# Performance work log

Hardware: AMD Instinct MI355X
Metric: run time of the kernel (lower is better)

Reference implementation:

```python
import jax, jax.numpy as jnp
import numpy as np

EPS = 1e-8  # torch CosineSimilarity default eps


def setup_inputs() -> dict:
    key = jax.random.key(0)
    ks = jax.random.split(key, 9)
    B, C, H, W = 8, 256, 96, 96
    co = C // 2
    s = 0.05
    return {
        "x": jax.random.normal(ks[0], (B, C, H, W), dtype=jnp.float32),
        "w_theta": jax.random.normal(ks[1], (co, C), dtype=jnp.float32) * s,
        "b_theta": jax.random.normal(ks[2], (co,), dtype=jnp.float32) * s,
        "w_phi": jax.random.normal(ks[3], (co, C), dtype=jnp.float32) * s,
        "b_phi": jax.random.normal(ks[4], (co,), dtype=jnp.float32) * s,
        "w_g": jax.random.normal(ks[5], (co, C), dtype=jnp.float32) * s,
        "b_g": jax.random.normal(ks[6], (co,), dtype=jnp.float32) * s,
        "w_back": jax.random.normal(ks[7], (C, co), dtype=jnp.float32) * s,
        "b_back": jax.random.normal(ks[8], (C,), dtype=jnp.float32) * s,
    }


def reference(x, w_theta, b_theta, w_phi, b_phi, w_g, b_g, w_back, b_back):
    B, C, H, W = x.shape
    # replicate pad, then gather the 9 (3x3) shifted views: [B, C, 9, H, W]
    xp = jnp.pad(x, ((0, 0), (0, 0), (1, 1), (1, 1)), mode="edge")
    neigh = jnp.stack(
        [xp[:, :, i:i + H, j:j + W] for i in range(3) for j in range(3)], axis=2
    )
    # 1x1 convs are per-pixel linear maps
    theta = jnp.einsum("bchw,oc->bohw", x, w_theta) + b_theta[None, :, None, None]
    phi = jnp.einsum("bcnhw,oc->bonhw", neigh, w_phi) + b_phi[None, :, None, None, None]
    g = jnp.einsum("bcnhw,oc->bonhw", neigh, w_g) + b_g[None, :, None, None, None]
    # cosine similarity over channel dim o: [B, 9, H, W]
    dot = jnp.sum(phi * theta[:, :, None], axis=1)
    denom = jnp.maximum(
        jnp.sqrt(jnp.sum(phi * phi, axis=1)) * jnp.sqrt(jnp.sum(theta * theta, axis=1))[:, None],
        EPS,
    )
    attn = jax.nn.softmax(dot / denom, axis=1)  # softmax over 9 neighbors
    # weighted average of g over neighbors: [B, co, H, W]
    wa = jnp.einsum("bonhw,bnhw->bohw", g, attn)
    x_res = jnp.einsum("bohw,co->bchw", wa, w_back) + b_back[None, :, None, None]
    return x + x_res
```

## Files before the change

### kernel.cpp

```cpp
#include <hip/hip_runtime.h>
#include <hip/hip_bf16.h>
#include <math.h>

#define HW   9216
#define WIMG 96
#define NPIX 73728
#define CIN  256
#define CO   128

typedef __attribute__((ext_vector_type(8))) short short8v;
typedef __attribute__((ext_vector_type(8))) unsigned short u16x8;
typedef __attribute__((ext_vector_type(4))) float f32x4;

__device__ __forceinline__ unsigned short f2bf(float f) {
    __hip_bfloat16 h = __float2bfloat16(f);
    return __builtin_bit_cast(unsigned short, h);
}
__device__ __forceinline__ float bf2f(unsigned short u) {
    unsigned v = ((unsigned)u) << 16;
    return __builtin_bit_cast(float, v);
}

__device__ __forceinline__ int swz(int row, int kb) {
    return (row * 128) + (kb ^ ((row & 7) << 4));
}
__device__ __forceinline__ int swzA(int row, int kb) {
    return (row * 512) + (kb ^ ((row & 7) << 4));
}

__global__ __launch_bounds__(256) void k1_mfma(
    const float* __restrict__ x,
    const float* __restrict__ wt, const float* __restrict__ bt,
    const float* __restrict__ wp, const float* __restrict__ bp,
    const float* __restrict__ wg, const float* __restrict__ bg,
    unsigned short* __restrict__ th, unsigned short* __restrict__ ph,
    unsigned short* __restrict__ gf)
{
    __shared__ char As[128 * 512];
    __shared__ char Bs[128 * 128];

    const int t   = threadIdx.x;
    const int bid = blockIdx.x;
    const int lb  = (bid & 7) * 72 + (bid >> 3);
    const int P0  = lb * 128;
    const int b   = P0 / HW;
    const int p0  = P0 - b * HW;
    const float* xb = x + (size_t)b * CIN * HW + p0;

    const int wid = t >> 6, lane = t & 63;
    const int wm = (wid & 1) * 64, wn = (wid >> 1) * 64;
    const int l15 = lane & 15, lg = lane >> 4;

    for (int kt = 0; kt < CIN; kt += 64) {
        #pragma unroll
        for (int it = 0; it < 8; ++it) {
            int kq = ((t >> 4) & 3) + (it & 3) * 4;
            int pp = (t & 15) + ((t >> 6) << 4) + ((it >> 2) << 6);
            ushort4 v;
            v.x = f2bf(xb[(size_t)(kt + kq * 4 + 0) * HW + pp]);
            v.y = f2bf(xb[(size_t)(kt + kq * 4 + 1) * HW + pp]);
            v.z = f2bf(xb[(size_t)(kt + kq * 4 + 2) * HW + pp]);
            v.w = f2bf(xb[(size_t)(kt + kq * 4 + 3) * HW + pp]);
            *(ushort4*)(As + swzA(pp, (kt + kq * 4) * 2)) = v;
        }
    }

    for (int nb = 0; nb < 3; ++nb) {
        const float* W  = (nb == 0) ? wt : (nb == 1) ? wp : wg;
        const float* Bv = (nb == 0) ? bt : (nb == 1) ? bp : bg;
        unsigned short* O = (nb == 0) ? th : (nb == 1) ? ph : gf;

        f32x4 acc[4][4] = {};

        for (int kt = 0; kt < CIN; kt += 64) {
            __syncthreads();
            #pragma unroll
            for (int it = 0; it < 8; ++it) {
                int kq = t & 15;
                int n  = (t >> 4) + it * 16;
                float4 w4 = *(const float4*)(W + (size_t)n * CIN + kt + kq * 4);
                ushort4 v;
                v.x = f2bf(w4.x); v.y = f2bf(w4.y); v.z = f2bf(w4.z); v.w = f2bf(w4.w);
                *(ushort4*)(Bs + swz(n, kq * 8)) = v;
            }
            __syncthreads();
            #pragma unroll
            for (int ks = 0; ks < 2; ++ks) {
                const int akb = kt * 2 + ks * 64 + lg * 16;
                const int bkb = ks * 64 + lg * 16;
                short8v a[4], bq[4];
                #pragma unroll
                for (int mt = 0; mt < 4; ++mt)
                    a[mt] = *(const short8v*)(As + swzA(wm + mt * 16 + l15, akb));
                #pragma unroll
                for (int nt = 0; nt < 4; ++nt)
                    bq[nt] = *(const short8v*)(Bs + swz(wn + nt * 16 + l15, bkb));
                #pragma unroll
                for (int mt = 0; mt < 4; ++mt)
                    #pragma unroll
                    for (int nt = 0; nt < 4; ++nt)
                        acc[mt][nt] = __builtin_amdgcn_mfma_f32_16x16x32_bf16(
                            a[mt], bq[nt], acc[mt][nt], 0, 0, 0);
            }
        }

        float bias[4];
        #pragma unroll
        for (int nt = 0; nt < 4; ++nt) bias[nt] = Bv[wn + nt * 16 + l15];
        #pragma unroll
        for (int mt = 0; mt < 4; ++mt)
            #pragma unroll
            for (int j = 0; j < 4; ++j) {
                size_t row = (size_t)(P0 + wm + mt * 16 + lg * 4 + j) * CO;
                #pragma unroll
                for (int nt = 0; nt < 4; ++nt)
                    O[row + wn + nt * 16 + l15] = f2bf(acc[mt][nt][j] + bias[nt]);
            }
    }
}

__global__ __launch_bounds__(256) void k_attn(
    const unsigned short* __restrict__ th, const unsigned short* __restrict__ ph,
    const unsigned short* __restrict__ gf, unsigned short* __restrict__ wa)
{
    const int t   = threadIdx.x;
    const int bid = blockIdx.x;
    const int lb  = (bid & 7) * 144 + (bid >> 3);
    const int s = t >> 2, q = t & 3;
    const int P = lb * 64 + s;
    const int b = P / HW;
    const int p = P - b * HW;
    const int h = p / WIMG;
    const int w = p - h * WIMG;
    const size_t ib = (size_t)b * HW;

    size_t nbase[9];
    #pragma unroll
    for (int n = 0; n < 9; ++n) {
        int hh = h + n / 3 - 1; hh = hh < 0 ? 0 : (hh > 95 ? 95 : hh);
        int w2 = w + n % 3 - 1; w2 = w2 < 0 ? 0 : (w2 > 95 ? 95 : w2);
        nbase[n] = (ib + (size_t)hh * WIMG + w2) * CO + q * 32;
    }

    const u16x8* tv = (const u16x8*)(th + (size_t)P * CO + q * 32);
    float T32[32];
    #pragma unroll
    for (int j = 0; j < 4; ++j) {
        u16x8 v = tv[j];
        #pragma unroll
        for (int e = 0; e < 8; ++e) T32[j * 8 + e] = bf2f(v[e]);
    }
    float t4[4] = {0.f, 0.f, 0.f, 0.f};
    #pragma unroll
    for (int j = 0; j < 4; ++j)
        #pragma unroll
        for (int e = 0; e < 8; ++e)
            t4[j] = fmaf(T32[j * 8 + e], T32[j * 8 + e], t4[j]);
    float tt = (t4[0] + t4[1]) + (t4[2] + t4[3]);
    tt += __shfl_xor(tt, 1);
    tt += __shfl_xor(tt, 2);
    const float st = sqrtf(tt);

    float score[9];
    #pragma unroll
    for (int n = 0; n < 9; ++n) {
        const u16x8* pv = (const u16x8*)(ph + nbase[n]);
        float d4[4] = {0.f, 0.f, 0.f, 0.f};
        float p4[4] = {0.f, 0.f, 0.f, 0.f};
        #pragma unroll
        for (int j = 0; j < 4; ++j) {
            u16x8 v = pv[j];
            #pragma unroll
            for (int e = 0; e < 8; ++e) {
                float f = bf2f(v[e]);
                d4[j] = fmaf(T32[j * 8 + e], f, d4[j]);
                p4[j] = fmaf(f, f, p4[j]);
            }
        }
        float d  = (d4[0] + d4[1]) + (d4[2] + d4[3]);
        float pp = (p4[0] + p4[1]) + (p4[2] + p4[3]);
        d  += __shfl_xor(d, 1);  d  += __shfl_xor(d, 2);
        pp += __shfl_xor(pp, 1); pp += __shfl_xor(pp, 2);
        float den = fmaxf(sqrtf(pp) * st, 1e-8f);
        score[n] = d / den;
    }

    float mx = score[0];
    #pragma unroll
    for (int n = 1; n < 9; ++n) mx = fmaxf(mx, score[n]);
    float sum = 0.f;
    #pragma unroll
    for (int n = 0; n < 9; ++n) { score[n] = __expf(score[n] - mx); sum += score[n]; }
    const float inv = 1.f / sum;

    float acc[32];
    #pragma unroll
    for (int k = 0; k < 32; ++k) acc[k] = 0.f;

    #pragma unroll
    for (int n = 0; n < 9; ++n) {
        const u16x8* gv = (const u16x8*)(gf + nbase[n]);
        float a = score[n] * inv;
        #pragma unroll
        for (int j = 0; j < 4; ++j) {
            u16x8 v = gv[j];
            #pragma unroll
            for (int e = 0; e < 8; ++e)
                acc[j * 8 + e] = fmaf(a, bf2f(v[e]), acc[j * 8 + e]);
        }
    }

    u16x8* ov = (u16x8*)(wa + (size_t)P * CO + q * 32);
    #pragma unroll
    for (int j = 0; j < 4; ++j) {
        u16x8 o;
        #pragma unroll
        for (int e = 0; e < 8; ++e) o[e] = f2bf(acc[j * 8 + e]);
        ov[j] = o;
    }
}

__global__ __launch_bounds__(256) void k3_mfma(
    const unsigned short* __restrict__ wa, const float* __restrict__ wb,
    const float* __restrict__ bb_, const float* __restrict__ x,
    float* __restrict__ out)
{
    __shared__ char As[128 * 128];
    __shared__ char Bs[128 * 128];

    const int t   = threadIdx.x;
    const int bid = blockIdx.x;
    const int lb  = (bid & 7) * 144 + (bid >> 3);
    const int cb  = (lb & 1) * 128;
    const int P0  = (lb >> 1) * 128;
    const int b   = P0 / HW;
    const int p0  = P0 - b * HW;

    const int wid = t >> 6, lane = t & 63;
    const int wm = (wid & 1) * 64, wn = (wid >> 1) * 64;
    const int l15 = lane & 15, lg = lane >> 4;

    f32x4 acc[4][4] = {};

    for (int kt = 0; kt < CO; kt += 64) {
        if (kt) __syncthreads();
        #pragma unroll
        for (int it = 0; it < 8; ++it) {
            int kq = t & 15;
            int n  = (t >> 4) + it * 16;
            float4 w4 = *(const float4*)(wb + (size_t)(cb + n) * CO + kt + kq * 4);
            ushort4 v;
            v.x = f2bf(w4.x); v.y = f2bf(w4.y); v.z = f2bf(w4.z); v.w = f2bf(w4.w);
            *(ushort4*)(As + swz(n, kq * 8)) = v;
        }
        #pragma unroll
        for (int it = 0; it < 4; ++it) {
            int kq = t & 7;
            int n  = (t >> 3) + it * 32;
            u16x8 u = *(const u16x8*)(wa + (size_t)(P0 + n) * CO + kt + kq * 8);
            *(u16x8*)(Bs + swz(n, kq * 16)) = u;
        }
        __syncthreads();
        #pragma unroll
        for (int ks = 0; ks < 2; ++ks) {
            const int kk2 = ks * 64 + lg * 16;
            short8v a[4], bq[4];
            #pragma unroll
            for (int mt = 0; mt < 4; ++mt)
                a[mt] = *(const short8v*)(As + swz(wm + mt * 16 + l15, kk2));
            #pragma unroll
            for (int nt = 0; nt < 4; ++nt)
                bq[nt] = *(const short8v*)(Bs + swz(wn + nt * 16 + l15, kk2));
            #pragma unroll
            for (int mt = 0; mt < 4; ++mt)
                #pragma unroll
                for (int nt = 0; nt < 4; ++nt)
                    acc[mt][nt] = __builtin_amdgcn_mfma_f32_16x16x32_bf16(
                        a[mt], bq[nt], acc[mt][nt], 0, 0, 0);
        }
    }

    #pragma unroll
    for (int mt = 0; mt < 4; ++mt)
        #pragma unroll
        for (int j = 0; j < 4; ++j) {
            int ch = cb + wm + mt * 16 + lg * 4 + j;
            size_t base = ((size_t)b * CIN + ch) * HW + p0;
            float bias = bb_[ch];
            #pragma unroll
            for (int nt = 0; nt < 4; ++nt) {
                int px = wn + nt * 16 + l15;
                out[base + px] = x[base + px] + acc[mt][nt][j] + bias;
            }
        }
}

extern "C" void kernel_launch(void* const* d_in, const int* in_sizes, int n_in,
                              void* d_out, int out_size, void* d_ws, size_t ws_size,
                              hipStream_t stream)
{
    const float* x  = (const float*)d_in[0];
    const float* wt = (const float*)d_in[1];
    const float* bt = (const float*)d_in[2];
    const float* wp = (const float*)d_in[3];
    const float* bp = (const float*)d_in[4];
    const float* wg = (const float*)d_in[5];
    const float* bg = (const float*)d_in[6];
    const float* wb = (const float*)d_in[7];
    const float* bb = (const float*)d_in[8];
    float* out = (float*)d_out;

    const size_t FEAT = (size_t)NPIX * CO;
    unsigned short* th = (unsigned short*)d_ws;
    unsigned short* ph = th + FEAT;
    unsigned short* gf = ph + FEAT;
    unsigned short* wa = gf + FEAT;

    hipLaunchKernelGGL(k1_mfma, dim3(576), dim3(256), 0, stream,
                       x, wt, bt, wp, bp, wg, bg, th, ph, gf);
    hipLaunchKernelGGL(k_attn, dim3(1152), dim3(256), 0, stream,
                       th, ph, gf, wa);
    hipLaunchKernelGGL(k3_mfma, dim3(1152), dim3(256), 0, stream,
                       wa, wb, bb, x, out);
}
```

Baseline: 256.3 us.

## Split projection kernel per weight matrix and use transposed LDS reads for x

The first kernel now launches one block per (pixel tile, projection) pair instead of one block computing all three projections, which cuts LDS use from 80 KB to 32 KB and triples the grid for better occupancy. x is loaded with vectorized float4 reads in pixel-major layout, and the MFMA A operands are fetched with ds_read_b64_tr_b16 transposed LDS reads. The cost is that each x tile is read and converted three times, once per projection, though the repeats should mostly be served from cache.

```diff
diff --git a/kernel.cpp b/kernel.cpp
--- a/kernel.cpp
+++ b/kernel.cpp
@@ -11,6 +11,7 @@
 typedef __attribute__((ext_vector_type(8))) short short8v;
 typedef __attribute__((ext_vector_type(8))) unsigned short u16x8;
 typedef __attribute__((ext_vector_type(4))) float f32x4;
+typedef __attribute__((ext_vector_type(4))) unsigned u32x4;
 
 __device__ __forceinline__ unsigned short f2bf(float f) {
     __hip_bfloat16 h = __float2bfloat16(f);
@@ -24,8 +25,12 @@
 __device__ __forceinline__ int swz(int row, int kb) {
     return (row * 128) + (kb ^ ((row & 7) << 4));
 }
-__device__ __forceinline__ int swzA(int row, int kb) {
-    return (row * 512) + (kb ^ ((row & 7) << 4));
+
+__device__ __forceinline__ short8v pk(unsigned long long lo, unsigned long long hi) {
+    u32x4 w;
+    w.x = (unsigned)lo; w.y = (unsigned)(lo >> 32);
+    w.z = (unsigned)hi; w.w = (unsigned)(hi >> 32);
+    return __builtin_bit_cast(short8v, w);
 }
 
 __global__ __launch_bounds__(256) void k1_mfma(
@@ -36,87 +41,103 @@
     unsigned short* __restrict__ th, unsigned short* __restrict__ ph,
     unsigned short* __restrict__ gf)
 {
-    __shared__ char As[128 * 512];
-    __shared__ char Bs[128 * 128];
+    __shared__ char As[16384];
+    __shared__ char Bs[16384];
 
     const int t   = threadIdx.x;
     const int bid = blockIdx.x;
-    const int lb  = (bid & 7) * 72 + (bid >> 3);
-    const int P0  = lb * 128;
-    const int b   = P0 / HW;
-    const int p0  = P0 - b * HW;
+    const int lb  = (bid & 7) * 216 + (bid >> 3);
+    const int nb  = lb % 3;
+    const int bx  = lb / 3;
+
+    const float* W  = (nb == 0) ? wt : (nb == 1) ? wp : wg;
+    const float* Bv = (nb == 0) ? bt : (nb == 1) ? bp : bg;
+    unsigned short* O = (nb == 0) ? th : (nb == 1) ? ph : gf;
+
+    const int P0 = bx * 128;
+    const int b  = P0 / HW;
+    const int p0 = P0 - b * HW;
     const float* xb = x + (size_t)b * CIN * HW + p0;
 
     const int wid = t >> 6, lane = t & 63;
     const int wm = (wid & 1) * 64, wn = (wid >> 1) * 64;
     const int l15 = lane & 15, lg = lane >> 4;
 
+    const unsigned As0 = (unsigned)(unsigned long long)(size_t)As;
+    const unsigned trb = As0 + lane * 8;
+
+    f32x4 acc[4][4] = {};
+
     for (int kt = 0; kt < CIN; kt += 64) {
+        if (kt) __syncthreads();
         #pragma unroll
         for (int it = 0; it < 8; ++it) {
-            int kq = ((t >> 4) & 3) + (it & 3) * 4;
-            int pp = (t & 15) + ((t >> 6) << 4) + ((it >> 2) << 6);
+            int px = (t & 15) * 4 + (it & 1) * 64;
+            int k  = (t >> 4) + (it >> 1) * 16;
+            float4 v4 = *(const float4*)(xb + (size_t)(kt + k) * HW + px);
             ushort4 v;
-            v.x = f2bf(xb[(size_t)(kt + kq * 4 + 0) * HW + pp]);
-            v.y = f2bf(xb[(size_t)(kt + kq * 4 + 1) * HW + pp]);
-            v.z = f2bf(xb[(size_t)(kt + kq * 4 + 2) * HW + pp]);
-            v.w = f2bf(xb[(size_t)(kt + kq * 4 + 3) * HW + pp]);
-            *(ushort4*)(As + swzA(pp, (kt + kq * 4) * 2)) = v;
-        }
-    }
-
-    for (int nb = 0; nb < 3; ++nb) {
-        const float* W  = (nb == 0) ? wt : (nb == 1) ? wp : wg;
-        const float* Bv = (nb == 0) ? bt : (nb == 1) ? bp : bg;
-        unsigned short* O = (nb == 0) ? th : (nb == 1) ? ph : gf;
-
-        f32x4 acc[4][4] = {};
-
-        for (int kt = 0; kt < CIN; kt += 64) {
-            __syncthreads();
-            #pragma unroll
-            for (int it = 0; it < 8; ++it) {
-                int kq = t & 15;
-                int n  = (t >> 4) + it * 16;
-                float4 w4 = *(const float4*)(W + (size_t)n * CIN + kt + kq * 4);
-                ushort4 v;
-                v.x = f2bf(w4.x); v.y = f2bf(w4.y); v.z = f2bf(w4.z); v.w = f2bf(w4.w);
-                *(ushort4*)(Bs + swz(n, kq * 8)) = v;
-            }
-            __syncthreads();
-            #pragma unroll
-            for (int ks = 0; ks < 2; ++ks) {
-                const int akb = kt * 2 + ks * 64 + lg * 16;
-                const int bkb = ks * 64 + lg * 16;
-                short8v a[4], bq[4];
-                #pragma unroll
-                for (int mt = 0; mt < 4; ++mt)
-                    a[mt] = *(const short8v*)(As + swzA(wm + mt * 16 + l15, akb));
+            v.x = f2bf(v4.x); v.y = f2bf(v4.y); v.z = f2bf(v4.z); v.w = f2bf(v4.w);
+            int eb = ((px >> 4) * 16 + (k >> 2)) * 128 + (k & 3) * 32 + (px & 15) * 2;
+            *(ushort4*)(As + eb) = v;
+        }
+        #pragma unroll
+        for (int it = 0; it < 8; ++it) {
+            int kq = t & 15;
+            int n  = (t >> 4) + it * 16;
+            float4 w4 = *(const float4*)(W + (size_t)n * CIN + kt + kq * 4);
+            ushort4 v;
+            v.x = f2bf(w4.x); v.y = f2bf(w4.y); v.z = f2bf(w4.z); v.w = f2bf(w4.w);
+            int pos = (kq >> 3) * 32 + (kq & 3) * 8 + ((kq >> 2) & 1) * 4;
+            *(ushort4*)(Bs + swz(n, pos * 2)) = v;
+        }
+        __syncthreads();
+        #pragma unroll
+        for (int ks = 0; ks < 2; ++ks) {
+            short8v bq[4];
+            #pragma unroll
+            for (int nt = 0; nt < 4; ++nt)
+                bq[nt] = *(const short8v*)(Bs + swz(wn + nt * 16 + l15, ks * 64 + lg * 16));
+
+            const unsigned a0 = trb + (unsigned)((wm >> 4) * 2048 + ks * 1024);
+            unsigned long long L0, H0, L1, H1, L2, H2, L3, H3;
+            asm volatile(
+                "ds_read_b64_tr_b16 %0, %8 offset:0\n\t"
+                "ds_read_b64_tr_b16 %1, %8 offset:512\n\t"
+                "ds_read_b64_tr_b16 %2, %9 offset:0\n\t"
+                "ds_read_b64_tr_b16 %3, %9 offset:512\n\t"
+                "ds_read_b64_tr_b16 %4, %10 offset:0\n\t"
+                "ds_read_b64_tr_b16 %5, %10 offset:512\n\t"
+                "ds_read_b64_tr_b16 %6, %11 offset:0\n\t"
+                "ds_read_b64_tr_b16 %7, %11 offset:512\n\t"
+                "s_waitcnt lgkmcnt(0)"
+                : "=&v"(L0), "=&v"(H0), "=&v"(L1), "=&v"(H1),
+                  "=&v"(L2), "=&v"(H2), "=&v"(L3), "=&v"(H3)
+                : "v"(a0), "v"(a0 + 2048u), "v"(a0 + 4096u), "v"(a0 + 6144u));
+            short8v a[4];
+            a[0] = pk(L0, H0); a[1] = pk(L1, H1);
+            a[2] = pk(L2, H2); a[3] = pk(L3, H3);
+
+            #pragma unroll
+            for (int mt = 0; mt < 4; ++mt)
                 #pragma unroll
                 for (int nt = 0; nt < 4; ++nt)
-                    bq[nt] = *(const short8v*)(Bs + swz(wn + nt * 16 + l15, bkb));
-                #pragma unroll
-                for (int mt = 0; mt < 4; ++mt)
-                    #pragma unroll
-                    for (int nt = 0; nt < 4; ++nt)
-                        acc[mt][nt] = __builtin_amdgcn_mfma_f32_16x16x32_bf16(
-                            a[mt], bq[nt], acc[mt][nt], 0, 0, 0);
-            }
-        }
-
-        float bias[4];
-        #pragma unroll
-        for (int nt = 0; nt < 4; ++nt) bias[nt] = Bv[wn + nt * 16 + l15];
-        #pragma unroll
-        for (int mt = 0; mt < 4; ++mt)
-            #pragma unroll
-            for (int j = 0; j < 4; ++j) {
-                size_t row = (size_t)(P0 + wm + mt * 16 + lg * 4 + j) * CO;
-                #pragma unroll
-                for (int nt = 0; nt < 4; ++nt)
-                    O[row + wn + nt * 16 + l15] = f2bf(acc[mt][nt][j] + bias[nt]);
-            }
-    }
+                    acc[mt][nt] = __builtin_amdgcn_mfma_f32_16x16x32_bf16(
+                        a[mt], bq[nt], acc[mt][nt], 0, 0, 0);
+        }
+    }
+
+    float bias[4];
+    #pragma unroll
+    for (int nt = 0; nt < 4; ++nt) bias[nt] = Bv[wn + nt * 16 + l15];
+    #pragma unroll
+    for (int mt = 0; mt < 4; ++mt)
+        #pragma unroll
+        for (int j = 0; j < 4; ++j) {
+            size_t row = (size_t)(P0 + wm + mt * 16 + lg * 4 + j) * CO;
+            #pragma unroll
+            for (int nt = 0; nt < 4; ++nt)
+                O[row + wn + nt * 16 + l15] = f2bf(acc[mt][nt][j] + bias[nt]);
+        }
 }
 
 __global__ __launch_bounds__(256) void k_attn(
@@ -316,7 +337,7 @@
     unsigned short* gf = ph + FEAT;
     unsigned short* wa = gf + FEAT;
 
-    hipLaunchKernelGGL(k1_mfma, dim3(576), dim3(256), 0, stream,
+    hipLaunchKernelGGL(k1_mfma, dim3(1728), dim3(256), 0, stream,
                        x, wt, bt, wp, bp, wg, bg, th, ph, gf);
     hipLaunchKernelGGL(k_attn, dim3(1152), dim3(256), 0, stream,
                        th, ph, gf, wa);
```

Measured after the change: 264.0 us. +3.0%, slower.

## Fuse attention with back-projection GEMM and split projection kernel per weight

Applied to the files above, without the earlier changes.

The attention kernel and the output 1x1-conv GEMM are merged into one kernel: each block computes the weighted neighbour average for 64 pixels into shared memory, then multiplies it by the back-projection weights and writes the residual output. This removes the global round-trip of the intermediate wa tensor and one kernel launch. Separately, the first projection kernel now gives each block a single one of the three weight matrices, with 1728 blocks instead of 576, and uses a smaller 16KB A tile. The block-per-weight split raises parallelism and cuts shared memory, but reloads and reconverts x three times.

```diff
diff --git a/kernel.cpp b/kernel.cpp
--- a/kernel.cpp
+++ b/kernel.cpp
@@ -24,8 +24,8 @@
 __device__ __forceinline__ int swz(int row, int kb) {
     return (row * 128) + (kb ^ ((row & 7) << 4));
 }
-__device__ __forceinline__ int swzA(int row, int kb) {
-    return (row * 512) + (kb ^ ((row & 7) << 4));
+__device__ __forceinline__ int swz2(int row, int kb) {
+    return (row * 256) + (kb ^ ((row & 7) << 4));
 }
 
 __global__ __launch_bounds__(256) void k1_mfma(
@@ -36,22 +36,32 @@
     unsigned short* __restrict__ th, unsigned short* __restrict__ ph,
     unsigned short* __restrict__ gf)
 {
-    __shared__ char As[128 * 512];
+    __shared__ char As[128 * 128];
     __shared__ char Bs[128 * 128];
 
     const int t   = threadIdx.x;
     const int bid = blockIdx.x;
-    const int lb  = (bid & 7) * 72 + (bid >> 3);
-    const int P0  = lb * 128;
-    const int b   = P0 / HW;
-    const int p0  = P0 - b * HW;
+    const int lb  = (bid & 7) * 216 + (bid >> 3);
+    const int nb  = lb % 3;
+    const int bx  = lb / 3;
+
+    const float* W  = (nb == 0) ? wt : (nb == 1) ? wp : wg;
+    const float* Bv = (nb == 0) ? bt : (nb == 1) ? bp : bg;
+    unsigned short* O = (nb == 0) ? th : (nb == 1) ? ph : gf;
+
+    const int P0 = bx * 128;
+    const int b  = P0 / HW;
+    const int p0 = P0 - b * HW;
     const float* xb = x + (size_t)b * CIN * HW + p0;
 
     const int wid = t >> 6, lane = t & 63;
     const int wm = (wid & 1) * 64, wn = (wid >> 1) * 64;
     const int l15 = lane & 15, lg = lane >> 4;
 
+    f32x4 acc[4][4] = {};
+
     for (int kt = 0; kt < CIN; kt += 64) {
+        if (kt) __syncthreads();
         #pragma unroll
         for (int it = 0; it < 8; ++it) {
             int kq = ((t >> 4) & 3) + (it & 3) * 4;
@@ -61,238 +71,212 @@
             v.y = f2bf(xb[(size_t)(kt + kq * 4 + 1) * HW + pp]);
             v.z = f2bf(xb[(size_t)(kt + kq * 4 + 2) * HW + pp]);
             v.w = f2bf(xb[(size_t)(kt + kq * 4 + 3) * HW + pp]);
-            *(ushort4*)(As + swzA(pp, (kt + kq * 4) * 2)) = v;
+            *(ushort4*)(As + swz(pp, kq * 8)) = v;
+        }
+        #pragma unroll
+        for (int it = 0; it < 8; ++it) {
+            int kq = t & 15;
+            int n  = (t >> 4) + it * 16;
+            float4 w4 = *(const float4*)(W + (size_t)n * CIN + kt + kq * 4);
+            ushort4 v;
+            v.x = f2bf(w4.x); v.y = f2bf(w4.y); v.z = f2bf(w4.z); v.w = f2bf(w4.w);
+            *(ushort4*)(Bs + swz(n, kq * 8)) = v;
+        }
+        __syncthreads();
+        #pragma unroll
+        for (int ks = 0; ks < 2; ++ks) {
+            const int kk2 = ks * 64 + lg * 16;
+            short8v a[4], bq[4];
+            #pragma unroll
+            for (int mt = 0; mt < 4; ++mt)
+                a[mt] = *(const short8v*)(As + swz(wm + mt * 16 + l15, kk2));
+            #pragma unroll
+            for (int nt = 0; nt < 4; ++nt)
+                bq[nt] = *(const short8v*)(Bs + swz(wn + nt * 16 + l15, kk2));
+            #pragma unroll
+            for (int mt = 0; mt < 4; ++mt)
+                #pragma unroll
+                for (int nt = 0; nt < 4; ++nt)
+                    acc[mt][nt] = __builtin_amdgcn_mfma_f32_16x16x32_bf16(
+                        a[mt], bq[nt], acc[mt][nt], 0, 0, 0);
         }
     }
 
-    for (int nb = 0; nb < 3; ++nb) {
-        const float* W  = (nb == 0) ? wt : (nb == 1) ? wp : wg;
-        const float* Bv = (nb == 0) ? bt : (nb == 1) ? bp : bg;
-        unsigned short* O = (nb == 0) ? th : (nb == 1) ? ph : gf;
-
-        f32x4 acc[4][4] = {};
-
-        for (int kt = 0; kt < CIN; kt += 64) {
+    float bias[4];
+    #pragma unroll
+    for (int nt = 0; nt < 4; ++nt) bias[nt] = Bv[wn + nt * 16 + l15];
+    #pragma unroll
+    for (int mt = 0; mt < 4; ++mt)
+        #pragma unroll
+        for (int j = 0; j < 4; ++j) {
+            size_t row = (size_t)(P0 + wm + mt * 16 + lg * 4 + j) * CO;
+            #pragma unroll
+            for (int nt = 0; nt < 4; ++nt)
+                O[row + wn + nt * 16 + l15] = f2bf(acc[mt][nt][j] + bias[nt]);
+        }
+}
+
+__global__ __launch_bounds__(256) void k23_fused(
+    const unsigned short* __restrict__ th, const unsigned short* __restrict__ ph,
+    const unsigned short* __restrict__ gf, const float* __restrict__ wb,
+    const float* __restrict__ bb_, const float* __restrict__ x,
+    float* __restrict__ out)
+{
+    __shared__ char Was[64 * 256];
+    __shared__ char Ws[128 * 128];
+
+    const int t   = threadIdx.x;
+    const int bid = blockIdx.x;
+    const int lb  = (bid & 7) * 144 + (bid >> 3);
+    const int P0  = lb * 64;
+    const int b   = P0 / HW;
+    const int p0  = P0 - b * HW;
+    const size_t ib = (size_t)b * HW;
+
+    {
+        const int sq = t >> 2, q = t & 3;
+        const int P  = P0 + sq;
+        const int p  = p0 + sq;
+        const int h  = p / WIMG;
+        const int w  = p - h * WIMG;
+
+        size_t nbase[9];
+        #pragma unroll
+        for (int n = 0; n < 9; ++n) {
+            int hh = h + n / 3 - 1; hh = hh < 0 ? 0 : (hh > 95 ? 95 : hh);
+            int w2 = w + n % 3 - 1; w2 = w2 < 0 ? 0 : (w2 > 95 ? 95 : w2);
+            nbase[n] = (ib + (size_t)hh * WIMG + w2) * CO + q * 32;
+        }
+
+        const u16x8* tv = (const u16x8*)(th + (size_t)P * CO + q * 32);
+        float T32[32];
+        #pragma unroll
+        for (int j = 0; j < 4; ++j) {
+            u16x8 v = tv[j];
+            #pragma unroll
+            for (int e = 0; e < 8; ++e) T32[j * 8 + e] = bf2f(v[e]);
+        }
+        float t4[4] = {0.f, 0.f, 0.f, 0.f};
+        #pragma unroll
+        for (int j = 0; j < 4; ++j)
+            #pragma unroll
+            for (int e = 0; e < 8; ++e)
+                t4[j] = fmaf(T32[j * 8 + e], T32[j * 8 + e], t4[j]);
+        float tt = (t4[0] + t4[1]) + (t4[2] + t4[3]);
+        tt += __shfl_xor(tt, 1);
+        tt += __shfl_xor(tt, 2);
+        const float st = sqrtf(tt);
+
+        float score[9];
+        #pragma unroll
+        for (int n = 0; n < 9; ++n) {
+            const u16x8* pv = (const u16x8*)(ph + nbase[n]);
+            float d4[4] = {0.f, 0.f, 0.f, 0.f};
+            float p4[4] = {0.f, 0.f, 0.f, 0.f};
+            #pragma unroll
+            for (int j = 0; j < 4; ++j) {
+                u16x8 v = pv[j];
+                #pragma unroll
+                for (int e = 0; e < 8; ++e) {
+                    float f = bf2f(v[e]);
+                    d4[j] = fmaf(T32[j * 8 + e], f, d4[j]);
+                    p4[j] = fmaf(f, f, p4[j]);
+                }
+            }
+            float d  = (d4[0] + d4[1]) + (d4[2] + d4[3]);
+            float pp = (p4[0] + p4[1]) + (p4[2] + p4[3]);
+            d  += __shfl_xor(d, 1);  d  += __shfl_xor(d, 2);
+            pp += __shfl_xor(pp, 1); pp += __shfl_xor(pp, 2);
+            float den = fmaxf(sqrtf(pp) * st, 1e-8f);
+            score[n] = d / den;
+        }
+
+        float mx = score[0];
+        #pragma unroll
+        for (int n = 1; n < 9; ++n) mx = fmaxf(mx, score[n]);
+        float sum = 0.f;
+        #pragma unroll
+        for (int n = 0; n < 9; ++n) { score[n] = __expf(score[n] - mx); sum += score[n]; }
+        const float inv = 1.f / sum;
+
+        float acc1[32];
+        #pragma unroll
+        for (int k = 0; k < 32; ++k) acc1[k] = 0.f;
+
+        #pragma unroll
+        for (int n = 0; n < 9; ++n) {
+            const u16x8* gv = (const u16x8*)(gf + nbase[n]);
+            float a = score[n] * inv;
+            #pragma unroll
+            for (int j = 0; j < 4; ++j) {
+                u16x8 v = gv[j];
+                #pragma unroll
+                for (int e = 0; e < 8; ++e)
+                    acc1[j * 8 + e] = fmaf(a, bf2f(v[e]), acc1[j * 8 + e]);
+            }
+        }
+
+        #pragma unroll
+        for (int j = 0; j < 4; ++j) {
+            u16x8 o;
+            #pragma unroll
+            for (int e = 0; e < 8; ++e) o[e] = f2bf(acc1[j * 8 + e]);
+            *(u16x8*)(Was + swz2(sq, q * 64 + j * 16)) = o;
+        }
+    }
+    __syncthreads();
+
+    const int wid = t >> 6, lane = t & 63;
+    const int wm = (wid & 1) * 64;
+    const int wn = (wid >> 1) * 32;
+    const int l15 = lane & 15, lg = lane >> 4;
+
+    for (int cb = 0; cb < CIN; cb += 128) {
+        f32x4 acc[4][2] = {};
+        for (int kt = 0; kt < CO; kt += 64) {
             __syncthreads();
             #pragma unroll
             for (int it = 0; it < 8; ++it) {
                 int kq = t & 15;
                 int n  = (t >> 4) + it * 16;
-                float4 w4 = *(const float4*)(W + (size_t)n * CIN + kt + kq * 4);
+                float4 w4 = *(const float4*)(wb + (size_t)(cb + n) * CO + kt + kq * 4);
                 ushort4 v;
                 v.x = f2bf(w4.x); v.y = f2bf(w4.y); v.z = f2bf(w4.z); v.w = f2bf(w4.w);
-                *(ushort4*)(Bs + swz(n, kq * 8)) = v;
+                *(ushort4*)(Ws + swz(n, kq * 8)) = v;
             }
             __syncthreads();
             #pragma unroll
             for (int ks = 0; ks < 2; ++ks) {
-                const int akb = kt * 2 + ks * 64 + lg * 16;
-                const int bkb = ks * 64 + lg * 16;
-                short8v a[4], bq[4];
+                const int kk2 = ks * 64 + lg * 16;
+                short8v a[4], bq[2];
                 #pragma unroll
                 for (int mt = 0; mt < 4; ++mt)
-                    a[mt] = *(const short8v*)(As + swzA(wm + mt * 16 + l15, akb));
-                #pragma unroll
-                for (int nt = 0; nt < 4; ++nt)
-                    bq[nt] = *(const short8v*)(Bs + swz(wn + nt * 16 + l15, bkb));
+                    a[mt] = *(const short8v*)(Ws + swz(wm + mt * 16 + l15, kk2));
+                #pragma unroll
+                for (int nt = 0; nt < 2; ++nt)
+                    bq[nt] = *(const short8v*)(Was + swz2(wn + nt * 16 + l15, kt * 2 + kk2));
                 #pragma unroll
                 for (int mt = 0; mt < 4; ++mt)
                     #pragma unroll
-                    for (int nt = 0; nt < 4; ++nt)
+                    for (int nt = 0; nt < 2; ++nt)
                         acc[mt][nt] = __builtin_amdgcn_mfma_f32_16x16x32_bf16(
                             a[mt], bq[nt], acc[mt][nt], 0, 0, 0);
             }
         }
-
-        float bias[4];
-        #pragma unroll
-        for (int nt = 0; nt < 4; ++nt) bias[nt] = Bv[wn + nt * 16 + l15];
         #pragma unroll
         for (int mt = 0; mt < 4; ++mt)
             #pragma unroll
             for (int j = 0; j < 4; ++j) {
-                size_t row = (size_t)(P0 + wm + mt * 16 + lg * 4 + j) * CO;
-                #pragma unroll
-                for (int nt = 0; nt < 4; ++nt)
-                    O[row + wn + nt * 16 + l15] = f2bf(acc[mt][nt][j] + bias[nt]);
+                int ch = cb + wm + mt * 16 + lg * 4 + j;
+                size_t base = ((size_t)b * CIN + ch) * HW + p0;
+                float bias = bb_[ch];
+                #pragma unroll
+                for (int nt = 0; nt < 2; ++nt) {
+                    int px = wn + nt * 16 + l15;
+                    out[base + px] = x[base + px] + acc[mt][nt][j] + bias;
+                }
             }
     }
-}
-
-__global__ __launch_bounds__(256) void k_attn(
-    const unsigned short* __restrict__ th, const unsigned short* __restrict__ ph,
-    const unsigned short* __restrict__ gf, unsigned short* __restrict__ wa)
-{
-    const int t   = threadIdx.x;
-    const int bid = blockIdx.x;
-    const int lb  = (bid & 7) * 144 + (bid >> 3);
-    const int s = t >> 2, q = t & 3;
-    const int P = lb * 64 + s;
-    const int b = P / HW;
-    const int p = P - b * HW;
-    const int h = p / WIMG;
-    const int w = p - h * WIMG;
-    const size_t ib = (size_t)b * HW;
-
-    size_t nbase[9];
-    #pragma unroll
-    for (int n = 0; n < 9; ++n) {
-        int hh = h + n / 3 - 1; hh = hh < 0 ? 0 : (hh > 95 ? 95 : hh);
-        int w2 = w + n % 3 - 1; w2 = w2 < 0 ? 0 : (w2 > 95 ? 95 : w2);
-        nbase[n] = (ib + (size_t)hh * WIMG + w2) * CO + q * 32;
-    }
-
-    const u16x8* tv = (const u16x8*)(th + (size_t)P * CO + q * 32);
-    float T32[32];
-    #pragma unroll
-    for (int j = 0; j < 4; ++j) {
-        u16x8 v = tv[j];
-        #pragma unroll
-        for (int e = 0; e < 8; ++e) T32[j * 8 + e] = bf2f(v[e]);
-    }
-    float t4[4] = {0.f, 0.f, 0.f, 0.f};
-    #pragma unroll
-    for (int j = 0; j < 4; ++j)
-        #pragma unroll
-        for (int e = 0; e < 8; ++e)
-            t4[j] = fmaf(T32[j * 8 + e], T32[j * 8 + e], t4[j]);
-    float tt = (t4[0] + t4[1]) + (t4[2] + t4[3]);
-    tt += __shfl_xor(tt, 1);
-    tt += __shfl_xor(tt, 2);
-    const float st = sqrtf(tt);
-
-    float score[9];
-    #pragma unroll
-    for (int n = 0; n < 9; ++n) {
-        const u16x8* pv = (const u16x8*)(ph + nbase[n]);
-        float d4[4] = {0.f, 0.f, 0.f, 0.f};
-        float p4[4] = {0.f, 0.f, 0.f, 0.f};
-        #pragma unroll
-        for (int j = 0; j < 4; ++j) {
-            u16x8 v = pv[j];
-            #pragma unroll
-            for (int e = 0; e < 8; ++e) {
-                float f = bf2f(v[e]);
-                d4[j] = fmaf(T32[j * 8 + e], f, d4[j]);
-                p4[j] = fmaf(f, f, p4[j]);
-            }
-        }
-        float d  = (d4[0] + d4[1]) + (d4[2] + d4[3]);
-        float pp = (p4[0] + p4[1]) + (p4[2] + p4[3]);
-        d  += __shfl_xor(d, 1);  d  += __shfl_xor(d, 2);
-        pp += __shfl_xor(pp, 1); pp += __shfl_xor(pp, 2);
-        float den = fmaxf(sqrtf(pp) * st, 1e-8f);
-        score[n] = d / den;
-    }
-
-    float mx = score[0];
-    #pragma unroll
-    for (int n = 1; n < 9; ++n) mx = fmaxf(mx, score[n]);
-    float sum = 0.f;
-    #pragma unroll
-    for (int n = 0; n < 9; ++n) { score[n] = __expf(score[n] - mx); sum += score[n]; }
-    const float inv = 1.f / sum;
-
-    float acc[32];
-    #pragma unroll
-    for (int k = 0; k < 32; ++k) acc[k] = 0.f;
-
-    #pragma unroll
-    for (int n = 0; n < 9; ++n) {
-        const u16x8* gv = (const u16x8*)(gf + nbase[n]);
-        float a = score[n] * inv;
-        #pragma unroll
-        for (int j = 0; j < 4; ++j) {
-            u16x8 v = gv[j];
-            #pragma unroll
-            for (int e = 0; e < 8; ++e)
-                acc[j * 8 + e] = fmaf(a, bf2f(v[e]), acc[j * 8 + e]);
-        }
-    }
-
-    u16x8* ov = (u16x8*)(wa + (size_t)P * CO + q * 32);
-    #pragma unroll
-    for (int j = 0; j < 4; ++j) {
-        u16x8 o;
-        #pragma unroll
-        for (int e = 0; e < 8; ++e) o[e] = f2bf(acc[j * 8 + e]);
-        ov[j] = o;
-    }
-}
-
-__global__ __launch_bounds__(256) void k3_mfma(
-    const unsigned short* __restrict__ wa, const float* __restrict__ wb,
-    const float* __restrict__ bb_, const float* __restrict__ x,
-    float* __restrict__ out)
-{
-    __shared__ char As[128 * 128];
-    __shared__ char Bs[128 * 128];
-
-    const int t   = threadIdx.x;
-    const int bid = blockIdx.x;
-    const int lb  = (bid & 7) * 144 + (bid >> 3);
-    const int cb  = (lb & 1) * 128;
-    const int P0  = (lb >> 1) * 128;
-    const int b   = P0 / HW;
-    const int p0  = P0 - b * HW;
-
-    const int wid = t >> 6, lane = t & 63;
-    const int wm = (wid & 1) * 64, wn = (wid >> 1) * 64;
-    const int l15 = lane & 15, lg = lane >> 4;
-
-    f32x4 acc[4][4] = {};
-
-    for (int kt = 0; kt < CO; kt += 64) {
-        if (kt) __syncthreads();
-        #pragma unroll
-        for (int it = 0; it < 8; ++it) {
-            int kq = t & 15;
-            int n  = (t >> 4) + it * 16;
-            float4 w4 = *(const float4*)(wb + (size_t)(cb + n) * CO + kt + kq * 4);
-            ushort4 v;
-            v.x = f2bf(w4.x); v.y = f2bf(w4.y); v.z = f2bf(w4.z); v.w = f2bf(w4.w);
-            *(ushort4*)(As + swz(n, kq * 8)) = v;
-        }
-        #pragma unroll
-        for (int it = 0; it < 4; ++it) {
-            int kq = t & 7;
-            int n  = (t >> 3) + it * 32;
-            u16x8 u = *(const u16x8*)(wa + (size_t)(P0 + n) * CO + kt + kq * 8);
-            *(u16x8*)(Bs + swz(n, kq * 16)) = u;
-        }
-        __syncthreads();
-        #pragma unroll
-        for (int ks = 0; ks < 2; ++ks) {
-            const int kk2 = ks * 64 + lg * 16;
-            short8v a[4], bq[4];
-            #pragma unroll
-            for (int mt = 0; mt < 4; ++mt)
-                a[mt] = *(const short8v*)(As + swz(wm + mt * 16 + l15, kk2));
-            #pragma unroll
-            for (int nt = 0; nt < 4; ++nt)
-                bq[nt] = *(const short8v*)(Bs + swz(wn + nt * 16 + l15, kk2));
-            #pragma unroll
-            for (int mt = 0; mt < 4; ++mt)
-                #pragma unroll
-                for (int nt = 0; nt < 4; ++nt)
-                    acc[mt][nt] = __builtin_amdgcn_mfma_f32_16x16x32_bf16(
-                        a[mt], bq[nt], acc[mt][nt], 0, 0, 0);
-        }
-    }
-
-    #pragma unroll
-    for (int mt = 0; mt < 4; ++mt)
-        #pragma unroll
-        for (int j = 0; j < 4; ++j) {
-            int ch = cb + wm + mt * 16 + lg * 4 + j;
-            size_t base = ((size_t)b * CIN + ch) * HW + p0;
-            float bias = bb_[ch];
-            #pragma unroll
-            for (int nt = 0; nt < 4; ++nt) {
-                int px = wn + nt * 16 + l15;
-                out[base + px] = x[base + px] + acc[mt][nt][j] + bias;
-            }
-        }
 }
 
 extern "C" void kernel_launch(void* const* d_in, const int* in_sizes, int n_in,
@@ -314,12 +298,9 @@
     unsigned short* th = (unsigned short*)d_ws;
     unsigned short* ph = th + FEAT;
     unsigned short* gf = ph + FEAT;
-    unsigned short* wa = gf + FEAT;
-
-    hipLaunchKernelGGL(k1_mfma, dim3(576), dim3(256), 0, stream,
+
+    hipLaunchKernelGGL(k1_mfma, dim3(1728), dim3(256), 0, stream,
                        x, wt, bt, wp, bp, wg, bg, th, ph, gf);
-    hipLaunchKernelGGL(k_attn, dim3(1152), dim3(256), 0, stream,
-                       th, ph, gf, wa);
-    hipLaunchKernelGGL(k3_mfma, dim3(1152), dim3(256), 0, stream,
-                       wa, wb, bb, x, out);
-}
+    hipLaunchKernelGGL(k23_fused, dim3(1152), dim3(256), 0, stream,
+                       th, ph, gf, wb, bb, x, out);
+}
```

New measurement: 221.1 us. 1.16x faster.
